# Kernel tuning notes

Hardware: AMD Instinct MI355X
Metric: run time of the kernel (lower is better)

The kernel has to match this reference:

```python
import jax, jax.numpy as jnp
import numpy as np

NA, NO = 3, 85  # anchors per level, nc+5
OUT = NA * NO   # 255


def _p(key, shape):
    return jax.random.normal(key, shape, dtype=jnp.float32) * 0.02


def setup_inputs() -> dict:
    key = jax.random.key(0)
    ks = jax.random.split(key, 12)
    return {
        'x0': jax.random.normal(ks[0], (8, 128, 160, 160), jnp.float32),
        'x1': jax.random.normal(ks[1], (8, 256, 80, 80), jnp.float32),
        'x2': jax.random.normal(ks[2], (8, 512, 40, 40), jnp.float32),
        'x3': jax.random.normal(ks[3], (8, 1024, 20, 20), jnp.float32),
        # CLLABlock 1x1 convs (weight stored as [out_ch, in_ch])
        'w_conv1': _p(ks[4], (128, 128)), 'b_conv1': jnp.zeros((128,), jnp.float32),
        'w_conv2': _p(ks[5], (128, 256)), 'b_conv2': jnp.zeros((128,), jnp.float32),
        # CLLA q/k/v Linear layers (torch Linear: [out_feat, in_feat])
        'wq': _p(ks[6], (128, 128)), 'bq': jnp.zeros((128,), jnp.float32),
        'wk': _p(ks[7], (128, 128)), 'bk': jnp.zeros((128,), jnp.float32),
        'wv': _p(ks[8], (128, 128)), 'bv': jnp.zeros((128,), jnp.float32),
        # det head conv and extra level convs m[0], m[1]
        'w_det': _p(ks[9], (OUT, 128)), 'b_det': jnp.zeros((OUT,), jnp.float32),
        'wm0': _p(ks[10], (OUT, 512)), 'bm0': jnp.zeros((OUT,), jnp.float32),
        'wm1': _p(ks[11], (OUT, 1024)), 'bm1': jnp.zeros((OUT,), jnp.float32),
    }


def _conv1x1(x, w, b):
    # x: [b,c,h,w], w: [o,c]
    return jnp.einsum('bchw,oc->bohw', x, w) + b[None, :, None, None]


def _clla(f1, f2, wq, bq, wk, bk, wv, bv):
    # f1: [b,c,2H,2W] (fine), f2: [b,c,H,W] (coarse); range=2 -> pad=0
    b, c, H, W = f2.shape
    # torch loop: local[n] = f1[..., i::2, j::2], n = i*2+j, stacked on a new axis,
    # then permute(0,3,4,2,1) -> [b,H,W,4,c]
    loc = f1.reshape(b, c, H, 2, W, 2).transpose(0, 2, 4, 3, 5, 1).reshape(b, H, W, 4, c)
    x2_ = f2.transpose(0, 2, 3, 1)              # [b,H,W,c]
    q = x2_ @ wq.T + bq                          # [b,H,W,c]
    k = loc @ wk.T + bk                          # [b,H,W,4,c]
    v = loc @ wv.T + bv                          # [b,H,W,4,c]
    dots = jnp.einsum('bhwc,bhwnc->bhwn', q, k) / 2.0  # /range
    irr = 2.0 * jnp.mean(dots, axis=-1, keepdims=True) - dots
    att = jax.nn.softmax(irr, axis=-1)           # [b,H,W,4]
    out = jnp.einsum('bhwn,bhwnc->bhwc', att, v).transpose(0, 3, 1, 2)  # [b,c,H,W]
    return (out + f2) / 2.0


def _reshape_head(p):
    bs, _, ny, nx = p.shape
    return p.reshape(bs, NA, NO, ny, nx).transpose(0, 1, 3, 4, 2)  # [bs,na,ny,nx,no]


def reference(x0, x1, x2, x3,
              w_conv1, b_conv1, w_conv2, b_conv2,
              wq, bq, wk, bk, wv, bv,
              w_det, b_det, wm0, bm0, wm1, bm1):
    # training-mode forward of CLLADetect: returns raw head outputs p
    f1 = _conv1x1(x0, w_conv1, b_conv1)
    f2 = _conv1x1(x1, w_conv2, b_conv2)
    f = _clla(f1, f2, wq, bq, wk, bk, wv, bv)
    p0 = _reshape_head(_conv1x1(f, w_det, b_det))   # [8,3,80,80,85]
    p1 = _reshape_head(_conv1x1(x2, wm0, bm0))      # [8,3,40,40,85]
    p2 = _reshape_head(_conv1x1(x3, wm1, bm1))      # [8,3,20,20,85]
    return (p0, p1, p2)
```

## Files before the change

kernel.cpp:

```cpp
#include <hip/hip_runtime.h>

typedef unsigned short u16;
typedef unsigned int   u32;
typedef __bf16 bf16x8 __attribute__((ext_vector_type(8)));
typedef float  f32x4  __attribute__((ext_vector_type(4)));

__device__ __forceinline__ u16 f2bf(float f){
  u32 u = __float_as_uint(f);
  return (u16)((u + 0x7FFFu + ((u >> 16) & 1u)) >> 16);
}
__device__ __forceinline__ float bf2f(u16 h){ return __uint_as_float(((u32)h) << 16); }

#define WS_A1    0u
#define WS_WM0   196608u
#define WS_WM1   458752u
#define WS_WDVC  983040u
#define WS_C1    1048576u
#define WS_B3    1050112u
#define WS_BM0   1051136u
#define WS_BM1   1052160u
#define WS_T     1053184u
#define WS_U     1184256u
#define WS_MR    1184768u
#define WS_CR    1315840u
#define WS_W6    1316352u
#define WS_U6    1381888u
#define WS_R     1382400u

__device__ __forceinline__ size_t wimg_off(int n, int k, int BN, int nK){
  int nt = n / BN, r = n % BN, kt = k >> 6;
  int slot = (((k & 63) >> 3) ^ (r & 7));
  return (size_t)(nt * nK + kt) * (size_t)(BN * 128) + (size_t)r * 128 + (slot << 4) + (k & 7) * 2;
}

__global__ __launch_bounds__(256) void prep1_k(const float* __restrict__ wq, const float* __restrict__ bq,
                                               const float* __restrict__ wc2, const float* __restrict__ bc2,
                                               char* ws)
{
  float* T = (float*)(ws + WS_T);
  float* u = (float*)(ws + WS_U);
  const int a = blockIdx.x, j = threadIdx.x;
  float s = 0.f;
  for (int c = 0; c < 128; c++) s += wq[a * 128 + c] * wc2[c * 256 + j];
  T[a * 256 + j] = s;
  if (j == 0){
    float su = bq[a];
    for (int c = 0; c < 128; c++) su += wq[a * 128 + c] * bc2[c];
    u[a] = su;
  }
}

__global__ __launch_bounds__(256) void prep1b_k(const float* __restrict__ wk,
                                                const float* __restrict__ wv,
                                                const float* __restrict__ wc1,
                                                const float* __restrict__ bc1,
                                                const float* __restrict__ bv,
                                                char* ws)
{
  const float* T = (const float*)(ws + WS_T);
  const float* u = (const float*)(ws + WS_U);
  const int blk = blockIdx.x, j = threadIdx.x;
  if (blk < 128){
    int n = blk;
    float s = 0.f;
    for (int a = 0; a < 128; a++) s += wk[a * 128 + n] * T[a * 256 + j];
    ((float*)(ws + WS_MR))[n * 256 + j] = 0.5f * s;
    if (j == 0){
      float sc = 0.f;
      for (int a = 0; a < 128; a++) sc += wk[a * 128 + n] * u[a];
      ((float*)(ws + WS_CR))[n] = 0.5f * sc;
    }
  } else {
    int n = blk - 128;
    if (j < 128){
      float s = 0.f;
      for (int c = 0; c < 128; c++) s += wv[n * 128 + c] * wc1[c * 128 + j];
      ((float*)(ws + WS_W6))[n * 128 + j] = s;
    }
    if (j == 0){
      float s = bv[n];
      for (int c = 0; c < 128; c++) s += wv[n * 128 + c] * bc1[c];
      ((float*)(ws + WS_U6))[n] = s;
    }
  }
}

__global__ __launch_bounds__(256) void prep2_k(
    const float* __restrict__ wc1, const float* __restrict__ wc2,
    const float* __restrict__ wdet, const float* __restrict__ bdet,
    const float* __restrict__ wm0, const float* __restrict__ bm0,
    const float* __restrict__ wm1, const float* __restrict__ bm1,
    const float* __restrict__ bc2, char* ws)
{
  const float* MR = (const float*)(ws + WS_MR);
  const float* CR = (const float*)(ws + WS_CR);
  const float* W6 = (const float*)(ws + WS_W6);
  const float* U6 = (const float*)(ws + WS_U6);
  int idx = blockIdx.x * 256 + threadIdx.x;
  if (idx < 98304){
    int n = idx >> 8, k = idx & 255;
    float s = 0.f;
    if (n < 128){
      for (int c = 0; c < 128; c++) s += wc1[c * 128 + n] * MR[c * 256 + k];
    } else if (n < 383){
      int oc = n - 128;
      for (int c = 0; c < 128; c++) s += wdet[oc * 128 + c] * wc2[c * 256 + k];
      s *= 0.5f;
    }
    *(u16*)(ws + WS_A1 + wimg_off(n, k, 128, 4)) = f2bf(s);
  } else if (idx < 98688){
    int n = idx - 98304;
    float s = 0.f;
    if (n < 128){
      for (int c = 0; c < 128; c++) s += wc1[c * 128 + n] * CR[c];
    }
    ((float*)(ws + WS_C1))[n] = s;
  } else if (idx < 131456){
    int id = idx - 98688; int n = id >> 7, k = id & 127;
    float s = 0.f;
    if (n < 255){
      for (int c = 0; c < 128; c++) s += wdet[n * 128 + c] * W6[c * 128 + k];
      s *= 0.5f;
    }
    ((u16*)(ws + WS_WDVC))[n * 128 + k] = f2bf(s);
  } else if (idx < 131712){
    int n = idx - 131456;
    float s = 0.f;
    if (n < 255){
      float ss = 0.f;
      for (int c = 0; c < 128; c++) ss += wdet[n * 128 + c] * U6[c];
      s = bdet[n] + 0.5f * ss;
    }
    ((float*)(ws + WS_B3))[n] = s;
  } else if (idx < 262784){
    int id = idx - 131712; int n = id >> 9, k = id & 511;
    float s = (n < 255) ? wm0[n * 512 + k] : 0.f;
    *(u16*)(ws + WS_WM0 + wimg_off(n, k, 256, 8)) = f2bf(s);
  } else if (idx < 524928){
    int id = idx - 262784; int n = id >> 10, k = id & 1023;
    float s = (n < 255) ? wm1[n * 1024 + k] : 0.f;
    *(u16*)(ws + WS_WM1 + wimg_off(n, k, 256, 16)) = f2bf(s);
  } else if (idx < 525440){
    int id = idx - 524928;
    if (id < 256) ((float*)(ws + WS_BM0))[id] = (id < 255) ? bm0[id] : 0.f;
    else { int n = id - 256; ((float*)(ws + WS_BM1))[n] = (n < 255) ? bm1[n] : 0.f; }
  } else if (idx < 525696){
    int n = idx - 525440;
    float s = 0.f;
    if (n < 255){
      for (int c = 0; c < 128; c++) s += wdet[n * 128 + c] * bc2[c];
    }
    ((float*)(ws + WS_C1))[128 + n] = 0.5f * s;
  }
}

template<int Kd, int BM, int BN, int WM, int WN, int PPB, int Cin, int EPI, int ROWB>
__device__ __forceinline__ void gemm_body(char* lds, int mt, int nt,
                                          const float* __restrict__ Ap, const char* __restrict__ wimg,
                                          const float* __restrict__ bias, void* __restrict__ outp, long out_off)
{
  constexpr int nK = Kd / 64;
  constexpr int NV = BM / 16;
  char* ldsA = lds;
  char* ldsW = lds + BM * 128;
  const int t = threadIdx.x;
  const int lane = t & 63;
  const int wid = t >> 6;
  const int wm = wid / WN, wn = wid % WN;
  const int m0 = mt * BM, n0 = nt * BN;
  const int lr = lane & 15, lg = lane >> 4;
  f32x4 acc[4][4] = {};

  const int q = t & 3, chl = t >> 2;
  const int chunkA = chl >> 3, elo = (chl & 7) * 2;

  for (int kt = 0; kt < nK; kt++){
    {
      const int c = kt * 64 + chl;
      float4 v4[NV];
      #pragma unroll
      for (int v = 0; v < NV; v++){
        int pg = m0 + v * 16 + q * 4;
        int bb = pg / PPB, pp = pg - bb * PPB;
        v4[v] = *(const float4*)(Ap + (size_t)bb * Cin * PPB + (size_t)c * PPB + pp);
      }
      #pragma unroll
      for (int v = 0; v < NV; v++){
        #pragma unroll
        for (int e = 0; e < 4; e++){
          int pi = v * 16 + q * 4 + e;
          float val = ((const float*)&v4[v])[e];
          *(u16*)(ldsA + pi * 128 + ((chunkA ^ (pi & 7)) << 4) + elo) = f2bf(val);
        }
      }
    }
    {
      const char* srct = wimg + (size_t)(nt * nK + kt) * (BN * 128);
      #pragma unroll
      for (int it = 0; it < BN / 32; it++){
        int off = t * 16 + it * 4096;
        *(uint4*)(ldsW + off) = *(const uint4*)(srct + off);
      }
    }
    __syncthreads();
    #pragma unroll
    for (int ks = 0; ks < 2; ks++){
      bf16x8 af[4], bfr[4];
      #pragma unroll
      for (int i = 0; i < 4; i++){
        int r = wm * 64 + i * 16 + lr;
        af[i] = *(const bf16x8*)(ldsA + r * 128 + ((((ks << 2) + lg) ^ (r & 7)) << 4));
      }
      #pragma unroll
      for (int j = 0; j < 4; j++){
        int r = wn * 64 + j * 16 + lr;
        bfr[j] = *(const bf16x8*)(ldsW + r * 128 + ((((ks << 2) + lg) ^ (r & 7)) << 4));
      }
      #pragma unroll
      for (int i = 0; i < 4; i++)
        #pragma unroll
        for (int j = 0; j < 4; j++)
          acc[i][j] = __builtin_amdgcn_mfma_f32_16x16x32_bf16(af[i], bfr[j], acc[i][j], 0, 0, 0);
    }
    __syncthreads();
  }

  if constexpr (EPI == 0){
    u16* lds2 = (u16*)lds;
    #pragma unroll
    for (int j = 0; j < 4; j++){
      int nl = wn * 64 + j * 16 + lr;
      float bs = bias[n0 + nl];
      #pragma unroll
      for (int i = 0; i < 4; i++){
        #pragma unroll
        for (int r = 0; r < 4; r++){
          int ml = wm * 64 + i * 16 + lg * 4 + r;
          lds2[ml * 136 + nl] = f2bf(acc[i][j][r] + bs);
        }
      }
    }
    __syncthreads();
    char* outb = (char*)outp;
    #pragma unroll
    for (int it = 0; it < BM / 16; it++){
      int idx = it * 256 + t;
      int row = idx >> 4, c16 = idx & 15;
      *(uint4*)(outb + (size_t)(m0 + row) * ROWB + n0 * 2 + c16 * 16) =
          *(const uint4*)((const char*)lds2 + row * 272 + c16 * 16);
    }
  } else {
    #pragma unroll
    for (int j = 0; j < 4; j++){
      int nn = n0 + wn * 64 + j * 16 + lr;
      float bs = bias[nn];
      #pragma unroll
      for (int i = 0; i < 4; i++){
        #pragma unroll
        for (int r = 0; r < 4; r++){
          int mm = m0 + wm * 64 + i * 16 + lg * 4 + r;
          float v = acc[i][j][r] + bs;
          if (nn < 255){
            int b = mm / PPB, p = mm - b * PPB;
            int a = nn / 85, o = nn - a * 85;
            ((float*)outp)[out_off + ((size_t)(b * 3 + a) * PPB + p) * 85 + o] = v;
          }
        }
      }
    }
  }
}

__global__ __launch_bounds__(256) void gemms_k(const float* __restrict__ x1,
                                               const float* __restrict__ x2,
                                               const float* __restrict__ x3,
                                               char* __restrict__ ws,
                                               float* __restrict__ out)
{
  __shared__ char lds[40960];
  const int bid = blockIdx.x;
  if (bid < 50){
    gemm_body<1024, 64, 256, 1, 4, 400, 1024, 2, 0>(lds, bid, 0,
        x3, ws + WS_WM1, (const float*)(ws + WS_BM1), out, 16320000L);
  } else if (bid < 250){
    gemm_body<512, 64, 256, 1, 4, 1600, 512, 2, 0>(lds, bid - 50, 0,
        x2, ws + WS_WM0, (const float*)(ws + WS_BM0), out, 13056000L);
  } else {
    int b2 = bid - 250;
    gemm_body<256, 128, 128, 2, 2, 6400, 256, 0, 768>(lds, b2 / 3, b2 % 3,
        x1, ws + WS_A1, (const float*)(ws + WS_C1), ws + WS_R, 0L);
  }
}

__global__ __launch_bounds__(256) void clla_k(const float* __restrict__ x0,
                                              const char* __restrict__ ws,
                                              float* __restrict__ out)
{
  __shared__ char smem[20480];
  char* x0s = smem;
  char* rs  = smem + 16384;
  float* stg = (float*)smem;

  const u16*  R    = (const u16*)(ws + WS_R);
  const char* Rb   = ws + WS_R;
  const char* wdvi = ws + WS_WDVC;
  const float* b3  = (const float*)(ws + WS_B3);

  const int t = threadIdx.x;
  const int lane = t & 63, wid = t >> 6;
  const int lr = lane & 15, lg = lane >> 4;
  const int blk = blockIdx.x;
  const int b = blk / 400, rem = blk % 400;
  const int h = rem / 5, w0 = (rem % 5) * 16;
  const int c0 = b * 6400 + h * 80 + w0;
  const int pr = h * 80 + w0;

  {
    const int ch = t >> 1, r = t & 1;
    const float* gp = x0 + ((size_t)b * 128 + ch) * 25600
                    + (size_t)(2 * h + r) * 160 + 2 * w0;
    float4 v4[8];
    #pragma unroll
    for (int i = 0; i < 8; i++) v4[i] = *(const float4*)(gp + i * 4);
    const int chunk = ch >> 3, elo = (ch & 7) * 2;
    #pragma unroll
    for (int i = 0; i < 8; i++){
      #pragma unroll
      for (int e = 0; e < 4; e++){
        int j = i * 4 + e;
        int fr = ((j >> 1) << 2) + r * 2 + (j & 1);
        float val = ((const float*)&v4[i])[e];
        *(u16*)(x0s + fr * 256 + (((chunk ^ ((fr & 7) << 1)) & 15) << 4) + elo) = f2bf(val);
      }
    }
    const int lc2 = t >> 4, c2 = t & 15;
    *(uint4*)(rs + lc2 * 256 + (((c2 ^ ((lc2 & 7) << 1)) & 15) << 4)) =
        *(const uint4*)(Rb + (size_t)(c0 + lc2) * 768 + c2 * 16);
  }
  __syncthreads();

  float myatt;
  {
    const int px = t >> 4, n = (t >> 2) & 3, cq2 = t & 3;
    const int fr = px * 4 + n;
    float d = 0.f;
    #pragma unroll
    for (int g = 0; g < 4; g++){
      int c = cq2 * 4 + g;
      bf16x8 rv = *(const bf16x8*)(rs  + px * 256 + (((c ^ ((px & 7) << 1)) & 15) << 4));
      bf16x8 fv = *(const bf16x8*)(x0s + fr * 256 + (((c ^ ((fr & 7) << 1)) & 15) << 4));
      #pragma unroll
      for (int e = 0; e < 8; e++) d += (float)rv[e] * (float)fv[e];
    }
    d += __shfl_xor(d, 1); d += __shfl_xor(d, 2);
    float s4 = d + __shfl_xor(d, 4); s4 += __shfl_xor(s4, 8);
    float irr = 0.5f * s4 - d;
    float mx = fmaxf(irr, __shfl_xor(irr, 4)); mx = fmaxf(mx, __shfl_xor(mx, 8));
    float e1 = __expf(irr - mx);
    float den = e1 + __shfl_xor(e1, 4); den += __shfl_xor(den, 8);
    myatt = e1 / den;
  }

  {
    const int px = t >> 4, cp = t & 15;
    float o[8];
    #pragma unroll
    for (int e = 0; e < 8; e++) o[e] = 0.f;
    #pragma unroll
    for (int n = 0; n < 4; n++){
      float a = __shfl(myatt, (t & 48) | (n << 2));
      int fr = px * 4 + n;
      bf16x8 fv = *(const bf16x8*)(x0s + fr * 256 + (((cp ^ ((fr & 7) << 1)) & 15) << 4));
      #pragma unroll
      for (int e = 0; e < 8; e++) o[e] += a * (float)fv[e];
    }
    uint4 wv_;
    wv_.x = (u32)f2bf(o[0]) | ((u32)f2bf(o[1]) << 16);
    wv_.y = (u32)f2bf(o[2]) | ((u32)f2bf(o[3]) << 16);
    wv_.z = (u32)f2bf(o[4]) | ((u32)f2bf(o[5]) << 16);
    wv_.w = (u32)f2bf(o[6]) | ((u32)f2bf(o[7]) << 16);
    *(uint4*)(rs + px * 256 + (((cp ^ ((px & 7) << 1)) & 15) << 4)) = wv_;
  }
  __syncthreads();

  {
    bf16x8 af[4];
    #pragma unroll
    for (int kt = 0; kt < 4; kt++){
      int chunk = kt * 4 + lg;
      af[kt] = *(const bf16x8*)(rs + lr * 256 + (((chunk ^ ((lr & 7) << 1)) & 15) << 4));
    }
    #pragma unroll
    for (int jj = 0; jj < 4; jj++){
      int jn = wid * 4 + jj;
      f32x4 acc = (f32x4){0.f, 0.f, 0.f, 0.f};
      #pragma unroll
      for (int kt = 0; kt < 4; kt++){
        bf16x8 bfr = *(const bf16x8*)(wdvi + (jn * 16 + lr) * 256 + (kt * 4 + lg) * 16);
        acc = __builtin_amdgcn_mfma_f32_16x16x32_bf16(af[kt], bfr, acc, 0, 0, 0);
      }
      int oc = jn * 16 + lr;
      if (oc < 255){
        int a = oc / 85, o = oc - a * 85;
        #pragma unroll
        for (int ri = 0; ri < 4; ri++){
          int px = lg * 4 + ri;
          float v = acc[ri] + bf2f(R[(size_t)(c0 + px) * 384 + 128 + oc]) + b3[oc];
          stg[a * 1360 + px * 85 + o] = v;
        }
      }
    }
  }
  __syncthreads();

  {
    #pragma unroll
    for (int it = 0; it < 16; it++){
      int idx = it * 256 + t;
      if (idx < 4080){
        int a = idx / 1360, r = idx - a * 1360;
        out[((size_t)(b * 3 + a) * 6400 + pr) * 85 + r] = stg[idx];
      }
    }
  }
}

extern "C" void kernel_launch(void* const* d_in, const int* in_sizes, int n_in,
                              void* d_out, int out_size, void* d_ws, size_t ws_size,
                              hipStream_t stream)
{
  (void)in_sizes; (void)n_in; (void)out_size; (void)ws_size;
  const float* x0  = (const float*)d_in[0];
  const float* x1  = (const float*)d_in[1];
  const float* x2  = (const float*)d_in[2];
  const float* x3  = (const float*)d_in[3];
  const float* wc1 = (const float*)d_in[4];  const float* bc1 = (const float*)d_in[5];
  const float* wc2 = (const float*)d_in[6];  const float* bc2 = (const float*)d_in[7];
  const float* wq  = (const float*)d_in[8];  const float* bq  = (const float*)d_in[9];
  const float* wk  = (const float*)d_in[10];
  const float* wv  = (const float*)d_in[12]; const float* bv  = (const float*)d_in[13];
  const float* wdt = (const float*)d_in[14]; const float* bdt = (const float*)d_in[15];
  const float* wm0 = (const float*)d_in[16]; const float* bm0 = (const float*)d_in[17];
  const float* wm1 = (const float*)d_in[18]; const float* bm1 = (const float*)d_in[19];
  char* ws = (char*)d_ws;
  float* out = (float*)d_out;

  prep1_k<<<128, 256, 0, stream>>>(wq, bq, wc2, bc2, ws);
  prep1b_k<<<256, 256, 0, stream>>>(wk, wv, wc1, bc1, bv, ws);
  prep2_k<<<2054, 256, 0, stream>>>(wc1, wc2, wdt, bdt, wm0, bm0, wm1, bm1, bc2, ws);
  gemms_k<<<1450, 256, 0, stream>>>(x1, x2, x3, ws, out);
  clla_k<<<3200, 256, 0, stream>>>(x0, ws, out);
}
```

Before: 138.5 us.

## Merge weight-prep kernels, fold det bias into GEMM, vectorize CLLA output stores

Reassociates the precomputed weight products so the two small prep kernels merge into one launch, cutting one kernel launch and a serial dependency. The det-head bias is folded into the GEMM bias vector C1, so the CLLA epilogue no longer reads a separate b3 array. The per-pixel head slice of R is staged into LDS with coalesced loads instead of scattered global reads. The final output writes become float4 stores. LDS use per block rises, which may lower occupancy.

```diff
diff --git a/kernel.cpp b/kernel.cpp
--- a/kernel.cpp
+++ b/kernel.cpp
@@ -16,13 +16,11 @@
 #define WS_WM1   458752u
 #define WS_WDVC  983040u
 #define WS_C1    1048576u
-#define WS_B3    1050112u
 #define WS_BM0   1051136u
 #define WS_BM1   1052160u
 #define WS_T     1053184u
 #define WS_U     1184256u
-#define WS_MR    1184768u
-#define WS_CR    1315840u
+#define WS_P     1184768u
 #define WS_W6    1316352u
 #define WS_U6    1381888u
 #define WS_R     1382400u
@@ -33,45 +31,32 @@
   return (size_t)(nt * nK + kt) * (size_t)(BN * 128) + (size_t)r * 128 + (slot << 4) + (k & 7) * 2;
 }
 
-__global__ __launch_bounds__(256) void prep1_k(const float* __restrict__ wq, const float* __restrict__ bq,
+__global__ __launch_bounds__(256) void prepA_k(const float* __restrict__ wq, const float* __restrict__ bq,
                                                const float* __restrict__ wc2, const float* __restrict__ bc2,
-                                               char* ws)
-{
-  float* T = (float*)(ws + WS_T);
-  float* u = (float*)(ws + WS_U);
-  const int a = blockIdx.x, j = threadIdx.x;
-  float s = 0.f;
-  for (int c = 0; c < 128; c++) s += wq[a * 128 + c] * wc2[c * 256 + j];
-  T[a * 256 + j] = s;
-  if (j == 0){
-    float su = bq[a];
-    for (int c = 0; c < 128; c++) su += wq[a * 128 + c] * bc2[c];
-    u[a] = su;
-  }
-}
-
-__global__ __launch_bounds__(256) void prep1b_k(const float* __restrict__ wk,
-                                                const float* __restrict__ wv,
-                                                const float* __restrict__ wc1,
-                                                const float* __restrict__ bc1,
-                                                const float* __restrict__ bv,
-                                                char* ws)
-{
-  const float* T = (const float*)(ws + WS_T);
-  const float* u = (const float*)(ws + WS_U);
+                                               const float* __restrict__ wk,  const float* __restrict__ wv,
+                                               const float* __restrict__ wc1, const float* __restrict__ bc1,
+                                               const float* __restrict__ bv,  char* ws)
+{
   const int blk = blockIdx.x, j = threadIdx.x;
   if (blk < 128){
-    int n = blk;
+    int a = blk;
     float s = 0.f;
-    for (int a = 0; a < 128; a++) s += wk[a * 128 + n] * T[a * 256 + j];
-    ((float*)(ws + WS_MR))[n * 256 + j] = 0.5f * s;
+    for (int c = 0; c < 128; c++) s += wq[a * 128 + c] * wc2[c * 256 + j];
+    ((float*)(ws + WS_T))[a * 256 + j] = s;
     if (j == 0){
-      float sc = 0.f;
-      for (int a = 0; a < 128; a++) sc += wk[a * 128 + n] * u[a];
-      ((float*)(ws + WS_CR))[n] = 0.5f * sc;
+      float su = bq[a];
+      for (int c = 0; c < 128; c++) su += wq[a * 128 + c] * bc2[c];
+      ((float*)(ws + WS_U))[a] = su;
+    }
+  } else if (blk < 256){
+    int n = blk - 128;
+    if (j < 128){
+      float s = 0.f;
+      for (int c = 0; c < 128; c++) s += wk[n * 128 + c] * wc1[c * 128 + j];
+      ((float*)(ws + WS_P))[n * 128 + j] = s;
     }
   } else {
-    int n = blk - 128;
+    int n = blk - 256;
     if (j < 128){
       float s = 0.f;
       for (int c = 0; c < 128; c++) s += wv[n * 128 + c] * wc1[c * 128 + j];
@@ -86,14 +71,15 @@
 }
 
 __global__ __launch_bounds__(256) void prep2_k(
-    const float* __restrict__ wc1, const float* __restrict__ wc2,
+    const float* __restrict__ wc2,
     const float* __restrict__ wdet, const float* __restrict__ bdet,
     const float* __restrict__ wm0, const float* __restrict__ bm0,
     const float* __restrict__ wm1, const float* __restrict__ bm1,
     const float* __restrict__ bc2, char* ws)
 {
-  const float* MR = (const float*)(ws + WS_MR);
-  const float* CR = (const float*)(ws + WS_CR);
+  const float* T  = (const float*)(ws + WS_T);
+  const float* u  = (const float*)(ws + WS_U);
+  const float* P  = (const float*)(ws + WS_P);
   const float* W6 = (const float*)(ws + WS_W6);
   const float* U6 = (const float*)(ws + WS_U6);
   int idx = blockIdx.x * 256 + threadIdx.x;
@@ -101,7 +87,8 @@
     int n = idx >> 8, k = idx & 255;
     float s = 0.f;
     if (n < 128){
-      for (int c = 0; c < 128; c++) s += wc1[c * 128 + n] * MR[c * 256 + k];
+      for (int i = 0; i < 128; i++) s += P[i * 128 + n] * T[i * 256 + k];
+      s *= 0.5f;
     } else if (n < 383){
       int oc = n - 128;
       for (int c = 0; c < 128; c++) s += wdet[oc * 128 + c] * wc2[c * 256 + k];
@@ -112,7 +99,13 @@
     int n = idx - 98304;
     float s = 0.f;
     if (n < 128){
-      for (int c = 0; c < 128; c++) s += wc1[c * 128 + n] * CR[c];
+      for (int i = 0; i < 128; i++) s += P[i * 128 + n] * u[i];
+      s *= 0.5f;
+    } else if (n < 383){
+      int oc = n - 128;
+      float ss = 0.f;
+      for (int c = 0; c < 128; c++) ss += wdet[oc * 128 + c] * (bc2[c] + U6[c]);
+      s = bdet[oc] + 0.5f * ss;
     }
     ((float*)(ws + WS_C1))[n] = s;
   } else if (idx < 131456){
@@ -123,34 +116,18 @@
       s *= 0.5f;
     }
     ((u16*)(ws + WS_WDVC))[n * 128 + k] = f2bf(s);
-  } else if (idx < 131712){
-    int n = idx - 131456;
-    float s = 0.f;
-    if (n < 255){
-      float ss = 0.f;
-      for (int c = 0; c < 128; c++) ss += wdet[n * 128 + c] * U6[c];
-      s = bdet[n] + 0.5f * ss;
-    }
-    ((float*)(ws + WS_B3))[n] = s;
-  } else if (idx < 262784){
-    int id = idx - 131712; int n = id >> 9, k = id & 511;
+  } else if (idx < 262528){
+    int id = idx - 131456; int n = id >> 9, k = id & 511;
     float s = (n < 255) ? wm0[n * 512 + k] : 0.f;
     *(u16*)(ws + WS_WM0 + wimg_off(n, k, 256, 8)) = f2bf(s);
-  } else if (idx < 524928){
-    int id = idx - 262784; int n = id >> 10, k = id & 1023;
+  } else if (idx < 524672){
+    int id = idx - 262528; int n = id >> 10, k = id & 1023;
     float s = (n < 255) ? wm1[n * 1024 + k] : 0.f;
     *(u16*)(ws + WS_WM1 + wimg_off(n, k, 256, 16)) = f2bf(s);
-  } else if (idx < 525440){
-    int id = idx - 524928;
+  } else if (idx < 525184){
+    int id = idx - 524672;
     if (id < 256) ((float*)(ws + WS_BM0))[id] = (id < 255) ? bm0[id] : 0.f;
     else { int n = id - 256; ((float*)(ws + WS_BM1))[n] = (n < 255) ? bm1[n] : 0.f; }
-  } else if (idx < 525696){
-    int n = idx - 525440;
-    float s = 0.f;
-    if (n < 255){
-      for (int c = 0; c < 128; c++) s += wdet[n * 128 + c] * bc2[c];
-    }
-    ((float*)(ws + WS_C1))[128 + n] = 0.5f * s;
   }
 }
 
@@ -296,15 +273,14 @@
                                               const char* __restrict__ ws,
                                               float* __restrict__ out)
 {
-  __shared__ char smem[20480];
+  __shared__ char smem[29184];
   char* x0s = smem;
   char* rs  = smem + 16384;
+  char* h0s = smem + 20480;
   float* stg = (float*)smem;
 
-  const u16*  R    = (const u16*)(ws + WS_R);
   const char* Rb   = ws + WS_R;
   const char* wdvi = ws + WS_WDVC;
-  const float* b3  = (const float*)(ws + WS_B3);
 
   const int t = threadIdx.x;
   const int lane = t & 63, wid = t >> 6;
@@ -336,6 +312,13 @@
     const int lc2 = t >> 4, c2 = t & 15;
     *(uint4*)(rs + lc2 * 256 + (((c2 ^ ((lc2 & 7) << 1)) & 15) << 4)) =
         *(const uint4*)(Rb + (size_t)(c0 + lc2) * 768 + c2 * 16);
+    #pragma unroll
+    for (int i = 0; i < 2; i++){
+      int idx = i * 256 + t;
+      int row = idx >> 5, c16 = idx & 31;
+      *(uint4*)(h0s + row * 544 + c16 * 16) =
+          *(const uint4*)(Rb + (size_t)(c0 + row) * 768 + 256 + c16 * 16);
+    }
   }
   __syncthreads();
 
@@ -405,7 +388,7 @@
         #pragma unroll
         for (int ri = 0; ri < 4; ri++){
           int px = lg * 4 + ri;
-          float v = acc[ri] + bf2f(R[(size_t)(c0 + px) * 384 + 128 + oc]) + b3[oc];
+          float v = acc[ri] + bf2f(*(const u16*)(h0s + px * 544 + oc * 2));
           stg[a * 1360 + px * 85 + o] = v;
         }
       }
@@ -415,11 +398,12 @@
 
   {
     #pragma unroll
-    for (int it = 0; it < 16; it++){
+    for (int it = 0; it < 4; it++){
       int idx = it * 256 + t;
-      if (idx < 4080){
-        int a = idx / 1360, r = idx - a * 1360;
-        out[((size_t)(b * 3 + a) * 6400 + pr) * 85 + r] = stg[idx];
+      if (idx < 1020){
+        int a = idx / 340, r4 = idx - a * 340;
+        *(float4*)(out + ((size_t)(b * 3 + a) * 6400 + pr) * 85 + r4 * 4) =
+            *(const float4*)(stg + a * 1360 + r4 * 4);
       }
     }
   }
@@ -445,9 +429,8 @@
   char* ws = (char*)d_ws;
   float* out = (float*)d_out;
 
-  prep1_k<<<128, 256, 0, stream>>>(wq, bq, wc2, bc2, ws);
-  prep1b_k<<<256, 256, 0, stream>>>(wk, wv, wc1, bc1, bv, ws);
-  prep2_k<<<2054, 256, 0, stream>>>(wc1, wc2, wdt, bdt, wm0, bm0, wm1, bm1, bc2, ws);
+  prepA_k<<<384, 256, 0, stream>>>(wq, bq, wc2, bc2, wk, wv, wc1, bc1, bv, ws);
+  prep2_k<<<2052, 256, 0, stream>>>(wc2, wdt, bdt, wm0, bm0, wm1, bm1, bc2, ws);
   gemms_k<<<1450, 256, 0, stream>>>(x1, x2, x3, ws, out);
   clla_k<<<3200, 256, 0, stream>>>(x0, ws, out);
 }
```

New measurement: 123.9 us. -10.5%, faster.
